# Kernel optimization log

Hardware: AMD Instinct MI355X
Metric: run time of the kernel (lower is better)

Reference implementation:

```python
import jax, jax.numpy as jnp
import numpy as np

N_QUBITS = 8
INPUT_DIM = 128
HIDDEN = 8
T = 512
B = 512


def _build_circuit_consts(n):
    # wire 0 is the most-significant bit of the 2^n basis index (torchquantum layout)
    dim = 1 << n
    idx = np.arange(dim)
    bits = (idx[:, None] >> (n - 1 - np.arange(n))) & 1          # [dim, n]
    zsign = (1 - 2 * bits).astype(np.float32)                     # <Z_w> signs, [dim, n]
    # compose CNOT(0,1)...CNOT(n-2,n-1), CNOT(n-1,0) into one permutation
    perm = idx.copy()
    pairs = [(i, i + 1) for i in range(n - 1)] + [(n - 1, 0)]
    for c, t in pairs:
        cmask = 1 << (n - 1 - c)
        tmask = 1 << (n - 1 - t)
        g = np.where(idx & cmask, idx ^ tmask, idx)               # flip target bit if control set
        perm = perm[g]
    return jnp.asarray(perm), jnp.asarray(zsign)

_PERM, _ZSIGN = _build_circuit_consts(N_QUBITS)


def _qlayer(z, theta):
    # RX(x) then RX(theta) on |0> per wire -> product state; CNOT ring permutes the
    # basis amplitudes, so probabilities permute; MeasureAll(PauliZ) = probs @ zsign.
    a = 0.5 * (z + theta[None, :])                                # [B, n]
    pq = jnp.stack([jnp.cos(a) ** 2, jnp.sin(a) ** 2], axis=-1)   # [B, n, 2]
    probs = pq[:, 0, :]
    for w in range(1, N_QUBITS):                                  # small fixed kron loop
        probs = (probs[:, :, None] * pq[:, w, None, :]).reshape(probs.shape[0], -1)
    probs = probs[:, _PERM]                                       # CNOT ring
    return probs @ _ZSIGN                                         # [B, n] expvals in [-1, 1]


def setup_inputs() -> dict:
    key = jax.random.key(0)
    ks = jax.random.split(key, 14)
    d_in = INPUT_DIM + HIDDEN
    mk_w = lambda k: jax.random.normal(k, (d_in, N_QUBITS), dtype=jnp.float32) * 0.05
    mk_t = lambda k: jax.random.normal(k, (N_QUBITS,), dtype=jnp.float32) * 0.1
    return {
        "inputs": jax.random.normal(ks[0], (T, B, INPUT_DIM), dtype=jnp.float32),
        "Wf": mk_w(ks[1]), "bf": jnp.zeros((N_QUBITS,), jnp.float32),
        "Wi": mk_w(ks[2]), "bi": jnp.zeros((N_QUBITS,), jnp.float32),
        "Wu": mk_w(ks[3]), "bu": jnp.zeros((N_QUBITS,), jnp.float32),
        "Wo": mk_w(ks[4]), "bo": jnp.zeros((N_QUBITS,), jnp.float32),
        "theta_f": mk_t(ks[5]), "theta_i": mk_t(ks[6]),
        "theta_u": mk_t(ks[7]), "theta_o": mk_t(ks[8]),
    }


def reference(inputs, Wf, bf, Wi, bi, Wu, bu, Wo, bo,
              theta_f, theta_i, theta_u, theta_o):
    hx0 = jnp.zeros((inputs.shape[1], HIDDEN), inputs.dtype)
    cx0 = jnp.zeros((inputs.shape[1], HIDDEN), inputs.dtype)

    def step(carry, x):
        hx, cx = carry
        comb = jnp.concatenate([x, hx], axis=1)                   # [B, D+H]
        f = jax.nn.sigmoid(_qlayer(comb @ Wf + bf, theta_f))
        i = jax.nn.sigmoid(_qlayer(comb @ Wi + bi, theta_i))
        g = jnp.tanh(_qlayer(comb @ Wu + bu, theta_u))
        o = jax.nn.sigmoid(_qlayer(comb @ Wo + bo, theta_o))
        cx = f * cx + i * g
        hx = o * jnp.tanh(cx)
        return (hx, cx), hx

    (hx, cx), outputs = jax.lax.scan(step, (hx0, cx0), inputs)
    return outputs, hx, cx
```

## Files before the change

### kernel.cpp

```cpp
#include <hip/hip_runtime.h>
#include <stdint.h>

#define T_STEPS 512
#define BATCH   512
#define IN_DIM  128
#define GDIM    32
#define SLICE   (BATCH * GDIM)
#define INV2PI  0.15915494309189535f

typedef float f4 __attribute__((ext_vector_type(4)));

template <int CTRL>
__device__ __forceinline__ float dppm(float x) {
    return __int_as_float(__builtin_amdgcn_mov_dpp(__float_as_int(x), CTRL, 0xF, 0xF, true));
}
template <int CTRL>
__device__ __forceinline__ float dppk(float old, float x) {
    return __int_as_float(__builtin_amdgcn_update_dpp(
        __float_as_int(old), __float_as_int(x), CTRL, 0xF, 0xF, false));
}

__device__ __forceinline__ float tanh_pade(float x) {
    float u = x * x;
    float n = fmaf(u, u + 105.0f, 945.0f);
    float d = fmaf(u, fmaf(u, 15.0f, 420.0f), 945.0f);
    return (x * n) * __builtin_amdgcn_rcpf(d);
}

__device__ __forceinline__ float tanh_poly1(float x) {
    float u = x * x;
    float h = fmaf(u, fmaf(u, fmaf(u, -0.0277f, 0.1204402f), -0.3310474f), 0.9999014f);
    return x * h;
}

__device__ __forceinline__ void gload_lds16(const float* g, float* l) {
    __builtin_amdgcn_global_load_lds(
        (const __attribute__((address_space(1))) void*)g,
        (__attribute__((address_space(3))) void*)l, 16, 0, 0);
}

__global__ __launch_bounds__(256) void qlstm_xproj(
    const float* __restrict__ inp,
    const float* __restrict__ Wf, const float* __restrict__ bf,
    const float* __restrict__ Wi, const float* __restrict__ bi,
    const float* __restrict__ Wu, const float* __restrict__ bu,
    const float* __restrict__ Wo, const float* __restrict__ bo,
    const float* __restrict__ thf, const float* __restrict__ thi,
    const float* __restrict__ thu, const float* __restrict__ tho,
    float* __restrict__ X)
{
    __shared__ float tile[64 * 129];
    const int tid = threadIdx.x;
    const long long row0 = (long long)blockIdx.x * 64;

    const f4* src = (const f4*)(inp + row0 * IN_DIM);
    #pragma unroll
    for (int i = 0; i < 8; ++i) {
        int f = tid + i * 256;
        f4 v = __builtin_nontemporal_load(src + f);
        int r = f >> 5, c = (f & 31) << 2;
        float* d = &tile[r * 129 + c];
        d[0] = v.x; d[1] = v.y; d[2] = v.z; d[3] = v.w;
    }
    __syncthreads();

    const int g  = __builtin_amdgcn_readfirstlane(tid >> 6);
    const int rl = tid & 63;

    const float* W  = (g == 0) ? Wf : (g == 1) ? Wi : (g == 2) ? Wu : Wo;
    const float* B  = (g == 0) ? bf : (g == 1) ? bi : (g == 2) ? bu : bo;
    const float* TH = (g == 0) ? thf : (g == 1) ? thi : (g == 2) ? thu : tho;

    float acc[8];
    #pragma unroll
    for (int j = 0; j < 8; ++j) acc[j] = B[j] + TH[j];

    #pragma unroll 8
    for (int k = 0; k < IN_DIM; ++k) {
        float v = tile[rl * 129 + k];
        #pragma unroll
        for (int j = 0; j < 8; ++j)
            acc[j] = fmaf(v, W[k * 8 + j], acc[j]);
    }

    float4* Xo = (float4*)(X + (row0 + rl) * GDIM + g * 8);
    Xo[0] = make_float4(acc[0] * INV2PI, acc[1] * INV2PI, acc[2] * INV2PI, acc[3] * INV2PI);
    Xo[1] = make_float4(acc[4] * INV2PI, acc[5] * INV2PI, acc[6] * INV2PI, acc[7] * INV2PI);
}

__global__ __launch_bounds__(64, 1) void qlstm_rec(
    const float* __restrict__ X,
    const float* __restrict__ Wf, const float* __restrict__ Wi,
    const float* __restrict__ Wu, const float* __restrict__ Wo,
    float* __restrict__ out)
{
    __shared__ float xb[2 * 2 * 128 * 32];

    const int lane = threadIdx.x;
    const int p    = lane & 15;
    const int q    = p >> 1;
    const int par  = lane & 1;
    const int s    = lane >> 5;
    const int bb   = (lane >> 4) & 1;
    const int qd   = (lane >> 2) & 3;
    const int gate = s * 2 + par;
    const int b    = blockIdx.x * 2 + bb;
    const int col  = s * 16 + par * 8 + q;

    const bool isq0   = (q == 0);
    const bool loHalf = (lane < 32);
    const bool sB     = (s == 1);
    const bool parB   = (par == 1);

    const float* Wg = (gate == 0) ? Wf : (gate == 1) ? Wi : (gate == 2) ? Wu : Wo;
    float wv[8];
    #pragma unroll
    for (int i = 0; i < 8; ++i)
        wv[i] = Wg[(IN_DIM + (i ^ (qd << 1))) * 8 + q] * INV2PI;

    const bool  isT = (gate == 2);
    const float sc  = isT ? 1.0f : 0.5f;
    const float aa  = isT ? 1.0f : 0.5f;
    const float bbv = isT ? 0.0f : 0.5f;

    const float* g0 = X + (lane >> 3) * SLICE + (lane & 7) * 4
                        + blockIdx.x * 2 * GDIM;
    auto stage = [&](int bi, int qs) {
        #pragma unroll
        for (int j = 0; j < 2; ++j) {
            float* dst = &xb[(bi * 2 + j) * 4096];
            const float* srcb = g0 + j * GDIM + qs * SLICE;
            #pragma unroll
            for (int n = 0; n < 16; ++n)
                gload_lds16(srcb + n * 8 * SLICE, dst + n * 256);
        }
    };

    stage(0, 0);
    asm volatile("s_waitcnt vmcnt(0)" ::: "memory");

    const float* xq0 = &xb[bb * 4096 + col];
    float xv0 = xq0[0];
    float xv1 = xq0[32];
    stage(1, 128);

    float hx = 0.0f, cx = 0.0f;
    const float ONE = 1.0f;
    float* outp = out + b * 8 + q;

    for (int qt = 0; qt < 4; ++qt) {
        const int bi = qt & 1;
        const float* xq = &xb[bi * 8192 + bb * 4096 + col];
        if (qt > 0) {
            asm volatile("s_waitcnt vmcnt(0)" ::: "memory");
            xv0 = xq[0];
            xv1 = xq[32];
            if (qt < 3) stage(1 - bi, (qt + 1) * 128);
        }

        auto qstep = [&](int t, int ls, float& XV) {
            float xv = XV;
            XV = xq[((ls + 2) & 127) * 32];

            float Ba = dppm<0x00>(hx);
            float Bb = dppm<0xAA>(hx);
            float Bc = dppm<0x141>(Ba);
            float Bd = dppm<0x141>(Bb);
            float Be = dppm<0x140>(Ba);
            float Bf = dppm<0x140>(Bb);
            float Bg = dppm<0x141>(Be);
            float Bk = dppm<0x141>(Bf);

            float mA = fmaf(Ba, wv[0], xv);
            mA = fmaf(Bb, wv[1], mA);
            mA = fmaf(Bc, wv[2], mA);
            mA = fmaf(Bd, wv[3], mA);
            float mB = Be * wv[6];
            mB = fmaf(Bf, wv[7], mB);
            mB = fmaf(Bg, wv[4], mB);
            mB = fmaf(Bk, wv[5], mB);
            float z = mA + mB;

            float cq = __builtin_amdgcn_cosf(z);

            float cc  = fabsf(cq) < 1e-30f ? 1e-30f : cq;
            float rcpc = __builtin_amdgcn_rcpf(cc);

            float P = cq * dppk<0x112>(ONE, cq);
            P = P * dppk<0x114>(ONE, P);
            P = P * dppk<0x118>(ONE, P);

            float Pm    = dppm<0x140>(P);
            float Pfull = dppm<0xB1>(Pm);
            float out0  = Pfull * rcpc;
            float outv  = isq0 ? out0 : P;

            float act = fmaf(tanh_poly1(outv * sc), aa, bbv);

            float n1 = dppm<0xB1>(act);
            auto pr = __builtin_amdgcn_permlane32_swap(
                __float_as_int(act), __float_as_int(act), false, false);
            float sw = __int_as_float(loHalf ? pr[1] : pr[0]);
            float sw2 = dppm<0xB1>(sw);

            float X1 = parB ? n1  : act;
            float X2 = parB ? act : n1;
            float Y1 = parB ? sw2 : sw;
            float Y2 = parB ? sw  : sw2;

            float fv = sB ? Y1 : X1;
            float iv = sB ? Y2 : X2;
            float uv = sB ? X1 : Y1;
            float ov = sB ? X2 : Y2;

            float ncx = fmaf(fv, cx, iv * uv);
            float nhx = ov * tanh_pade(ncx);
            cx = ncx;
            hx = nhx;

            __builtin_nontemporal_store(nhx, outp + t * (BATCH * 8));
        };

        #pragma unroll 2
        for (int ls = 0; ls < 128; ls += 2) {
            qstep(qt * 128 + ls,     ls,     xv0);
            qstep(qt * 128 + ls + 1, ls + 1, xv1);
        }
    }

    __builtin_nontemporal_store(hx, out + T_STEPS * BATCH * 8 + b * 8 + q);
    __builtin_nontemporal_store(cx, out + T_STEPS * BATCH * 8 + (BATCH + b) * 8 + q);
}

extern "C" void kernel_launch(void* const* d_in, const int* in_sizes, int n_in,
                              void* d_out, int out_size, void* d_ws, size_t ws_size,
                              hipStream_t stream) {
    const float* inp = (const float*)d_in[0];
    const float* Wf  = (const float*)d_in[1];
    const float* bf  = (const float*)d_in[2];
    const float* Wi  = (const float*)d_in[3];
    const float* bi  = (const float*)d_in[4];
    const float* Wu  = (const float*)d_in[5];
    const float* bu  = (const float*)d_in[6];
    const float* Wo  = (const float*)d_in[7];
    const float* bo  = (const float*)d_in[8];
    const float* thf = (const float*)d_in[9];
    const float* thi = (const float*)d_in[10];
    const float* thu = (const float*)d_in[11];
    const float* tho = (const float*)d_in[12];

    float* X   = (float*)d_ws;
    float* out = (float*)d_out;

    qlstm_xproj<<<(T_STEPS * BATCH) / 64, 256, 0, stream>>>(
        inp, Wf, bf, Wi, bi, Wu, bu, Wo, bo, thf, thi, thu, tho, X);

    qlstm_rec<<<BATCH / 2, 64, 0, stream>>>(X, Wf, Wi, Wu, Wo, out);
}
```

Before: 130.6 us.

## Make xproj persistent over 8 tiles with double-buffered LDS prefetch

Each xproj block now processes 8 consecutive 64-row tiles instead of one, and loads the next tile from global memory into registers while computing the current one, then writes it into a second LDS buffer. The aim is to hide global load latency behind the FMA loop and cut block launch overhead. In exchange the grid shrinks 8x (4096 to 512 blocks), LDS use doubles and register pressure rises, which may lower occupancy and parallelism on a GPU with many CUs.

```diff
diff --git a/kernel.cpp b/kernel.cpp
--- a/kernel.cpp
+++ b/kernel.cpp
@@ -49,43 +49,75 @@
     const float* __restrict__ thu, const float* __restrict__ tho,
     float* __restrict__ X)
 {
-    __shared__ float tile[64 * 129];
+    __shared__ float tile[2][64 * 129];
     const int tid = threadIdx.x;
-    const long long row0 = (long long)blockIdx.x * 64;
-
-    const f4* src = (const f4*)(inp + row0 * IN_DIM);
-    #pragma unroll
-    for (int i = 0; i < 8; ++i) {
-        int f = tid + i * 256;
-        f4 v = __builtin_nontemporal_load(src + f);
-        int r = f >> 5, c = (f & 31) << 2;
-        float* d = &tile[r * 129 + c];
-        d[0] = v.x; d[1] = v.y; d[2] = v.z; d[3] = v.w;
-    }
-    __syncthreads();
-
-    const int g  = __builtin_amdgcn_readfirstlane(tid >> 6);
-    const int rl = tid & 63;
+    const int g   = __builtin_amdgcn_readfirstlane(tid >> 6);
+    const int rl  = tid & 63;
+    const int t0  = blockIdx.x * 8;
 
     const float* W  = (g == 0) ? Wf : (g == 1) ? Wi : (g == 2) ? Wu : Wo;
     const float* B  = (g == 0) ? bf : (g == 1) ? bi : (g == 2) ? bu : bo;
     const float* TH = (g == 0) ? thf : (g == 1) ? thi : (g == 2) ? thu : tho;
 
-    float acc[8];
+    float binit[8];
     #pragma unroll
-    for (int j = 0; j < 8; ++j) acc[j] = B[j] + TH[j];
-
-    #pragma unroll 8
-    for (int k = 0; k < IN_DIM; ++k) {
-        float v = tile[rl * 129 + k];
-        #pragma unroll
-        for (int j = 0; j < 8; ++j)
-            acc[j] = fmaf(v, W[k * 8 + j], acc[j]);
+    for (int j = 0; j < 8; ++j) binit[j] = B[j] + TH[j];
+
+    f4 v[8];
+    {
+        const f4* src0 = (const f4*)(inp + (long long)t0 * 64 * IN_DIM);
+        #pragma unroll
+        for (int i = 0; i < 8; ++i)
+            v[i] = __builtin_nontemporal_load(src0 + tid + i * 256);
+        #pragma unroll
+        for (int i = 0; i < 8; ++i) {
+            int f = tid + i * 256;
+            int r = f >> 5, c = (f & 31) << 2;
+            float* d = &tile[0][r * 129 + c];
+            d[0] = v[i].x; d[1] = v[i].y; d[2] = v[i].z; d[3] = v[i].w;
+        }
     }
 
-    float4* Xo = (float4*)(X + (row0 + rl) * GDIM + g * 8);
-    Xo[0] = make_float4(acc[0] * INV2PI, acc[1] * INV2PI, acc[2] * INV2PI, acc[3] * INV2PI);
-    Xo[1] = make_float4(acc[4] * INV2PI, acc[5] * INV2PI, acc[6] * INV2PI, acc[7] * INV2PI);
+    for (int ti = 0; ti < 8; ++ti) {
+        const int cur = ti & 1;
+        __syncthreads();
+
+        if (ti < 7) {
+            const f4* srcn = (const f4*)(inp + (long long)(t0 + ti + 1) * 64 * IN_DIM);
+            #pragma unroll
+            for (int i = 0; i < 8; ++i)
+                v[i] = __builtin_nontemporal_load(srcn + tid + i * 256);
+        }
+        __builtin_amdgcn_sched_barrier(0);
+
+        float acc[8];
+        #pragma unroll
+        for (int j = 0; j < 8; ++j) acc[j] = binit[j];
+
+        const float* trow = &tile[cur][rl * 129];
+        #pragma unroll 8
+        for (int k = 0; k < IN_DIM; ++k) {
+            float x = trow[k];
+            #pragma unroll
+            for (int j = 0; j < 8; ++j)
+                acc[j] = fmaf(x, W[k * 8 + j], acc[j]);
+        }
+
+        long long row0 = (long long)(t0 + ti) * 64;
+        float4* Xo = (float4*)(X + (row0 + rl) * GDIM + g * 8);
+        Xo[0] = make_float4(acc[0] * INV2PI, acc[1] * INV2PI, acc[2] * INV2PI, acc[3] * INV2PI);
+        Xo[1] = make_float4(acc[4] * INV2PI, acc[5] * INV2PI, acc[6] * INV2PI, acc[7] * INV2PI);
+
+        if (ti < 7) {
+            #pragma unroll
+            for (int i = 0; i < 8; ++i) {
+                int f = tid + i * 256;
+                int r = f >> 5, c = (f & 31) << 2;
+                float* d = &tile[cur ^ 1][r * 129 + c];
+                d[0] = v[i].x; d[1] = v[i].y; d[2] = v[i].z; d[3] = v[i].w;
+            }
+        }
+    }
 }
 
 __global__ __launch_bounds__(64, 1) void qlstm_rec(
@@ -252,7 +284,7 @@
     float* X   = (float*)d_ws;
     float* out = (float*)d_out;
 
-    qlstm_xproj<<<(T_STEPS * BATCH) / 64, 256, 0, stream>>>(
+    qlstm_xproj<<<(T_STEPS * BATCH) / (64 * 8), 256, 0, stream>>>(
         inp, Wf, bf, Wi, bi, Wu, bu, Wo, bo, thf, thi, thu, tho, X);
 
     qlstm_rec<<<BATCH / 2, 64, 0, stream>>>(X, Wf, Wi, Wu, Wo, out);
```

Result: no change. 132.7 us (+1.6%).

## Compute all four gate projections per thread directly from global rows, drop LDS tile

Applied to the files above, without the earlier changes.

The input projection kernel changes from 256-thread blocks, which staged a 64-row tile in LDS and split the four gates across wavefronts, to 64-thread blocks. In the new version each thread reads its own input row with vector loads and accumulates all 32 gate outputs in registers. This removes the LDS staging, the barrier and the repeated LDS reads of each row by four wavefronts. In exchange, each lane's row loads are strided 512 bytes apart (uncoalesced), register pressure grows to 32 accumulators, and block-level parallelism drops.

```diff
diff --git a/kernel.cpp b/kernel.cpp
--- a/kernel.cpp
+++ b/kernel.cpp
@@ -39,7 +39,7 @@
         (__attribute__((address_space(3))) void*)l, 16, 0, 0);
 }
 
-__global__ __launch_bounds__(256) void qlstm_xproj(
+__global__ __launch_bounds__(64) void qlstm_xproj(
     const float* __restrict__ inp,
     const float* __restrict__ Wf, const float* __restrict__ bf,
     const float* __restrict__ Wi, const float* __restrict__ bi,
@@ -49,43 +49,45 @@
     const float* __restrict__ thu, const float* __restrict__ tho,
     float* __restrict__ X)
 {
-    __shared__ float tile[64 * 129];
-    const int tid = threadIdx.x;
-    const long long row0 = (long long)blockIdx.x * 64;
-
-    const f4* src = (const f4*)(inp + row0 * IN_DIM);
+    const int rl = threadIdx.x;
+    const long long row = (long long)blockIdx.x * 64 + rl;
+    const f4* rowp = (const f4*)(inp + row * IN_DIM);
+
+    float af[8], ai[8], au[8], ao[8];
     #pragma unroll
-    for (int i = 0; i < 8; ++i) {
-        int f = tid + i * 256;
-        f4 v = __builtin_nontemporal_load(src + f);
-        int r = f >> 5, c = (f & 31) << 2;
-        float* d = &tile[r * 129 + c];
-        d[0] = v.x; d[1] = v.y; d[2] = v.z; d[3] = v.w;
+    for (int j = 0; j < 8; ++j) {
+        af[j] = bf[j] + thf[j];
+        ai[j] = bi[j] + thi[j];
+        au[j] = bu[j] + thu[j];
+        ao[j] = bo[j] + tho[j];
     }
-    __syncthreads();
-
-    const int g  = __builtin_amdgcn_readfirstlane(tid >> 6);
-    const int rl = tid & 63;
-
-    const float* W  = (g == 0) ? Wf : (g == 1) ? Wi : (g == 2) ? Wu : Wo;
-    const float* B  = (g == 0) ? bf : (g == 1) ? bi : (g == 2) ? bu : bo;
-    const float* TH = (g == 0) ? thf : (g == 1) ? thi : (g == 2) ? thu : tho;
-
-    float acc[8];
-    #pragma unroll
-    for (int j = 0; j < 8; ++j) acc[j] = B[j] + TH[j];
-
-    #pragma unroll 8
-    for (int k = 0; k < IN_DIM; ++k) {
-        float v = tile[rl * 129 + k];
+
+    #pragma unroll 4
+    for (int kc = 0; kc < 32; ++kc) {
+        f4 v = __builtin_nontemporal_load(rowp + kc);
         #pragma unroll
-        for (int j = 0; j < 8; ++j)
-            acc[j] = fmaf(v, W[k * 8 + j], acc[j]);
+        for (int e = 0; e < 4; ++e) {
+            const int k = kc * 4 + e;
+            const float x = v[e];
+            #pragma unroll
+            for (int j = 0; j < 8; ++j) {
+                af[j] = fmaf(x, Wf[k * 8 + j], af[j]);
+                ai[j] = fmaf(x, Wi[k * 8 + j], ai[j]);
+                au[j] = fmaf(x, Wu[k * 8 + j], au[j]);
+                ao[j] = fmaf(x, Wo[k * 8 + j], ao[j]);
+            }
+        }
     }
 
-    float4* Xo = (float4*)(X + (row0 + rl) * GDIM + g * 8);
-    Xo[0] = make_float4(acc[0] * INV2PI, acc[1] * INV2PI, acc[2] * INV2PI, acc[3] * INV2PI);
-    Xo[1] = make_float4(acc[4] * INV2PI, acc[5] * INV2PI, acc[6] * INV2PI, acc[7] * INV2PI);
+    float4* Xo = (float4*)(X + row * GDIM);
+    Xo[0] = make_float4(af[0] * INV2PI, af[1] * INV2PI, af[2] * INV2PI, af[3] * INV2PI);
+    Xo[1] = make_float4(af[4] * INV2PI, af[5] * INV2PI, af[6] * INV2PI, af[7] * INV2PI);
+    Xo[2] = make_float4(ai[0] * INV2PI, ai[1] * INV2PI, ai[2] * INV2PI, ai[3] * INV2PI);
+    Xo[3] = make_float4(ai[4] * INV2PI, ai[5] * INV2PI, ai[6] * INV2PI, ai[7] * INV2PI);
+    Xo[4] = make_float4(au[0] * INV2PI, au[1] * INV2PI, au[2] * INV2PI, au[3] * INV2PI);
+    Xo[5] = make_float4(au[4] * INV2PI, au[5] * INV2PI, au[6] * INV2PI, au[7] * INV2PI);
+    Xo[6] = make_float4(ao[0] * INV2PI, ao[1] * INV2PI, ao[2] * INV2PI, ao[3] * INV2PI);
+    Xo[7] = make_float4(ao[4] * INV2PI, ao[5] * INV2PI, ao[6] * INV2PI, ao[7] * INV2PI);
 }
 
 __global__ __launch_bounds__(64, 1) void qlstm_rec(
@@ -252,7 +254,7 @@
     float* X   = (float*)d_ws;
     float* out = (float*)d_out;
 
-    qlstm_xproj<<<(T_STEPS * BATCH) / 64, 256, 0, stream>>>(
+    qlstm_xproj<<<(T_STEPS * BATCH) / 64, 64, 0, stream>>>(
         inp, Wf, bf, Wi, bi, Wu, bu, Wo, bo, thf, thi, thu, tho, X);
 
     qlstm_rec<<<BATCH / 2, 64, 0, stream>>>(X, Wf, Wi, Wu, Wo, out);
```

After: 173.5 us. 1.33x slower.
